# Kernel optimization log

Hardware: AMD Instinct MI355X
Metric: run time of the kernel (lower is better)

Reference implementation:

```python
import jax, jax.numpy as jnp
import numpy as np

B, S, D = 8, 2048, 512


def setup_inputs() -> dict:
    key = jax.random.key(0)
    ks = jax.random.split(key, 8)
    x = jax.random.normal(ks[0], (B, S, D), dtype=jnp.float32)
    mask = jax.random.randint(ks[1], (B, S, 1), 0, 2, dtype=jnp.int32)
    Wq = jax.random.normal(ks[2], (D, D), dtype=jnp.float32) / np.sqrt(D)
    bq = jax.random.normal(ks[3], (D,), dtype=jnp.float32) * 0.01
    Wk = jax.random.normal(ks[4], (D, D), dtype=jnp.float32) / np.sqrt(D)
    bk = jax.random.normal(ks[5], (D,), dtype=jnp.float32) * 0.01
    Wv = jax.random.normal(ks[6], (D, D), dtype=jnp.float32) / np.sqrt(D)
    bv = jax.random.normal(ks[7], (D,), dtype=jnp.float32) * 0.01
    return {"x": x, "mask": mask, "Wq": Wq, "bq": bq, "Wk": Wk, "bk": bk, "Wv": Wv, "bv": bv}


def reference(x, mask, Wq, bq, Wk, bk, Wv, bv):
    # torch Linear: y = x @ W^T + b
    Q = jnp.einsum('bsd,ed->bse', x, Wq) + bq
    K = jnp.einsum('bsd,ed->bse', x, Wk) + bk
    V = jnp.einsum('bsd,ed->bse', x, Wv) + bv
    scale = 1.0 / jnp.sqrt(jnp.asarray(x.shape[-1], dtype=x.dtype))
    scores = jnp.einsum('bqd,bkd->bqk', Q, K) * scale  # [B, S, S]
    attn_mask = jnp.transpose(mask, (0, 2, 1))  # [B, 1, S], broadcasts over queries
    scores = jnp.where(attn_mask == 0, jnp.asarray(-10000.0, dtype=scores.dtype), scores)
    attn = jax.nn.softmax(scores, axis=-1)
    return jnp.einsum('bqk,bkd->bqd', attn, V)
```

## Files before the change

kernel.cpp:

```cpp
#include <hip/hip_runtime.h>
#include <cstddef>

#define BB 8
#define SS 2048
#define DD 512
#define MM (BB * SS)

typedef __attribute__((ext_vector_type(8))) short bf16x8;
typedef __attribute__((ext_vector_type(4))) float f32x4;
typedef __attribute__((ext_vector_type(4))) unsigned short u16x4;

__device__ __forceinline__ f32x4 mfma16(bf16x8 a, bf16x8 b, f32x4 c) {
  return __builtin_amdgcn_mfma_f32_16x16x32_bf16(a, b, c, 0, 0, 0);
}
__device__ __forceinline__ unsigned short f2bf(float f) {
  unsigned int u = __float_as_uint(f);
  u += 0x7fffu + ((u >> 16) & 1u);
  return (unsigned short)(u >> 16);
}
__device__ __forceinline__ void gld16(const void* g, void* l) {
  __builtin_amdgcn_global_load_lds((const __attribute__((address_space(1))) void*)g,
                                   (__attribute__((address_space(3))) void*)l, 16, 0, 0);
}

__global__ void prep_kernel(const float* __restrict__ x, unsigned short* __restrict__ Xb,
                            const float* __restrict__ Wq, const float* __restrict__ Wk,
                            const float* __restrict__ Wv, unsigned short* __restrict__ Wqb,
                            unsigned short* __restrict__ Wkb, unsigned short* __restrict__ Wvb,
                            const int* __restrict__ mask, int* __restrict__ idx,
                            int* __restrict__ nbArr) {
  __shared__ int part[256];
  const int bx = blockIdx.x;
  const int t = threadIdx.x;
  if (bx < 8192) {
    const int i = bx * 256 + t;
    f32x4 v = reinterpret_cast<const f32x4*>(x)[i];
    u16x4 o;
    o[0] = f2bf(v[0]);
    o[1] = f2bf(v[1]);
    o[2] = f2bf(v[2]);
    o[3] = f2bf(v[3]);
    reinterpret_cast<u16x4*>(Xb)[i] = o;
    return;
  }
  if (bx < 8960) {
    const int k = bx - 8192;
    const int which = k >> 8;
    const float* s = which == 0 ? Wq : (which == 1 ? Wk : Wv);
    unsigned short* d = which == 0 ? Wqb : (which == 1 ? Wkb : Wvb);
    const int i = (k & 255) * 256 + t;
    f32x4 v = reinterpret_cast<const f32x4*>(s)[i];
    u16x4 o;
    o[0] = f2bf(v[0]);
    o[1] = f2bf(v[1]);
    o[2] = f2bf(v[2]);
    o[3] = f2bf(v[3]);
    reinterpret_cast<u16x4*>(d)[i] = o;
    return;
  }
  const int b = bx - 8960;
  int m[8], c = 0;
#pragma unroll
  for (int e = 0; e < 8; ++e) {
    m[e] = mask[b * SS + t * 8 + e];
    c += (m[e] != 0);
  }
  int v = c;
  part[t] = v;
  __syncthreads();
  for (int off = 1; off < 256; off <<= 1) {
    int u = (t >= off) ? part[t - off] : 0;
    __syncthreads();
    v += u;
    part[t] = v;
    __syncthreads();
  }
  int base = v - c;
#pragma unroll
  for (int e = 0; e < 8; ++e)
    if (m[e]) idx[b * SS + base++] = t * 8 + e;
  const int nb = part[255];
  if (t == 255) nbArr[b] = nb;
  for (int j = nb + t; j < SS; j += 256) idx[b * SS + j] = 0;
}

__global__ __launch_bounds__(256, 2) void qkv_gemm_kernel(
    const unsigned short* __restrict__ X, const unsigned short* __restrict__ W0,
    const unsigned short* __restrict__ W1, const unsigned short* __restrict__ W2,
    const float* __restrict__ b0, const float* __restrict__ b1,
    const float* __restrict__ b2, unsigned short* __restrict__ O0,
    unsigned short* __restrict__ O1, unsigned short* __restrict__ O2) {
  __shared__ unsigned char a_lds[2][128 * 128];
  __shared__ unsigned char b_lds[2][128 * 128];
  const int tid = threadIdx.x;
  const int w = tid >> 6, l = tid & 63, lr = l & 15, hi = l >> 4;
  const int bid = blockIdx.x;
  const int xcd = bid & 7;
  const int rest = bid >> 3;
  const int j = rest % 12;
  const int mhi = rest / 12;
  const int which = j >> 2;
  const unsigned short* W = which == 0 ? W0 : (which == 1 ? W1 : W2);
  const float* bias = which == 0 ? b0 : (which == 1 ? b1 : b2);
  unsigned short* out = which == 0 ? O0 : (which == 1 ? O1 : O2);
  const float oscale = which == 0 ? 0.044194173824159216f : 1.0f;
  const int m0 = ((mhi << 3) | xcd) * 128;
  const int n0 = (j & 3) * 128;
  const int wm = (w >> 1) * 64, wn = (w & 1) * 64;
  const int srow = l >> 3, gchunk = (l & 7) ^ (srow & 7);

  f32x4 acc[4][4];
#pragma unroll
  for (int mt = 0; mt < 4; ++mt)
#pragma unroll
    for (int nt = 0; nt < 4; ++nt) acc[mt][nt] = (f32x4){0.f, 0.f, 0.f, 0.f};

  const unsigned short* ga = X + (size_t)(m0 + w * 32 + srow) * DD + gchunk * 8;
  const unsigned short* gb = W + (size_t)(n0 + w * 32 + srow) * DD + gchunk * 8;

  for (int k0 = 0; k0 < DD; k0 += 128) {
#pragma unroll
    for (int ii = 0; ii < 4; ++ii) {
      gld16(ga + (size_t)ii * 8 * DD + k0, &a_lds[0][(w * 4 + ii) * 1024]);
      gld16(gb + (size_t)ii * 8 * DD + k0, &b_lds[0][(w * 4 + ii) * 1024]);
      gld16(ga + (size_t)ii * 8 * DD + k0 + 64, &a_lds[1][(w * 4 + ii) * 1024]);
      gld16(gb + (size_t)ii * 8 * DD + k0 + 64, &b_lds[1][(w * 4 + ii) * 1024]);
    }
    __syncthreads();
#pragma unroll
    for (int hf = 0; hf < 2; ++hf) {
#pragma unroll
      for (int dkl = 0; dkl < 2; ++dkl) {
        const int gc = dkl * 4 + hi;
        bf16x8 af[4], bfr[4];
#pragma unroll
        for (int mt = 0; mt < 4; ++mt) {
          const int row = wm + mt * 16 + lr;
          af[mt] = *reinterpret_cast<const bf16x8*>(
              &a_lds[hf][row * 128 + ((gc ^ (row & 7)) * 16)]);
        }
#pragma unroll
        for (int nt = 0; nt < 4; ++nt) {
          const int row = wn + nt * 16 + lr;
          bfr[nt] = *reinterpret_cast<const bf16x8*>(
              &b_lds[hf][row * 128 + ((gc ^ (row & 7)) * 16)]);
        }
#pragma unroll
        for (int mt = 0; mt < 4; ++mt)
#pragma unroll
          for (int nt = 0; nt < 4; ++nt)
            acc[mt][nt] = mfma16(af[mt], bfr[nt], acc[mt][nt]);
      }
    }
    __syncthreads();
  }

#pragma unroll
  for (int nt = 0; nt < 4; ++nt) {
    const int col = n0 + wn + nt * 16 + lr;
    const float bv = bias[col];
#pragma unroll
    for (int mt = 0; mt < 4; ++mt)
#pragma unroll
      for (int r = 0; r < 4; ++r) {
        const int row = m0 + wm + mt * 16 + hi * 4 + r;
        out[(size_t)row * DD + col] = f2bf((acc[mt][nt][r] + bv) * oscale);
      }
  }
}

__global__ void vtrans_kernel(const unsigned short* __restrict__ V,
                              const int* __restrict__ idx, const int* __restrict__ nbArr,
                              unsigned short* __restrict__ VT2) {
  __shared__ unsigned short t[64][72];
  const int b = blockIdx.z;
  const int kt = blockIdx.x;
  const int d0 = blockIdx.y * 64;
  const int tid = threadIdx.x;
  const int c = tid & 63, rg = tid >> 6;
  const int nb = nbArr[b];
#pragma unroll
  for (int i = 0; i < 16; ++i) {
    const int row = rg * 16 + i;
    const int s = kt * 64 + row;
    const int src = s < nb ? idx[b * SS + s] : 0;
    t[row][c] = V[((size_t)b * SS + src) * DD + d0 + c];
  }
  __syncthreads();
#pragma unroll
  for (int i = 0; i < 16; ++i) {
    const int ix = i * 256 + tid;
    const int jj = ix & 7;
    const int dl = (ix >> 3) & 63;
    const int cc = ix >> 9;
    VT2[(((size_t)(b * 32 + kt) * 8 + cc) * 512 + d0 + dl) * 8 + jj] =
        t[cc * 8 + jj][dl];
  }
}

__global__ __launch_bounds__(256, 2) void attn_kernel(
    const unsigned short* __restrict__ Q, const unsigned short* __restrict__ K,
    const unsigned short* __restrict__ VT2, const int* __restrict__ idx,
    const int* __restrict__ nbArr, float* __restrict__ Out,
    float* __restrict__ Apart, float* __restrict__ mlpart) {
  __shared__ unsigned char k_lds[32 * 1024];
  __shared__ unsigned char vt_lds[4 * 512 * 16];
  __shared__ unsigned short pbuf[4][16][32];
  __shared__ int ids[1024];
  const int tid = threadIdx.x;
  const int w = tid >> 6, l = tid & 63, lr = l & 15, hi = l >> 4;
  const int bid = blockIdx.x;
  const int b = bid & 7;
  const int qt = (bid >> 3) >> 1;
  const int sp = (bid >> 3) & 1;
  const int q0 = qt * 64 + w * 16;

  const int nb = nbArr[b];
  const int ntile = (nb + 31) >> 5;
  const int half = (ntile + 1) >> 1;
  const int lo = sp == 0 ? 0 : half;
  const int hi_t = sp == 0 ? half : ntile;
  const int ntl = hi_t - lo;

  const unsigned short* __restrict__ Qb = Q + (size_t)b * SS * DD;
  const unsigned short* __restrict__ Kb = K + (size_t)b * SS * DD;
  const unsigned short* __restrict__ Vb = VT2 + (size_t)b * SS * DD;
  const int* __restrict__ idxb = idx + b * SS;

  for (int j = tid; j < ntl * 32; j += 256) ids[j] = idxb[lo * 32 + j];

  bf16x8 qf[16];
#pragma unroll
  for (int dk = 0; dk < 16; ++dk)
    qf[dk] = *reinterpret_cast<const bf16x8*>(
        &Qb[(size_t)(q0 + lr) * DD + dk * 32 + hi * 8]);

  f32x4 oacc[32];
#pragma unroll
  for (int i = 0; i < 32; ++i) oacc[i] = (f32x4){0.f, 0.f, 0.f, 0.f};
  float mrow[4], lrow[4];
#pragma unroll
  for (int r = 0; r < 4; ++r) {
    mrow[r] = -10000.0f;
    lrow[r] = 0.0f;
  }

  __syncthreads();

  for (int t = lo; t < hi_t; ++t) {
    const int tr = t - lo;
#pragma unroll
    for (int r = 0; r < 8; ++r) {
      const int row = w * 8 + r;
      const int src = ids[tr * 32 + row];
      const int ch = (l & 56) | ((l ^ row) & 7);
      gld16(Kb + (size_t)src * DD + ch * 8, &k_lds[row * 1024]);
    }
    const size_t vbase = ((size_t)((t >> 1) * 8 + (t & 1) * 4 + w) * 512);
#pragma unroll
    for (int g = 0; g < 8; ++g)
      gld16(Vb + (vbase + g * 64 + l) * 8, &vt_lds[(w * 512 + g * 64) * 16]);

    asm volatile("s_waitcnt vmcnt(8)" ::: "memory");
    __builtin_amdgcn_s_barrier();

    f32x4 sacc[2];
#pragma unroll
    for (int nt = 0; nt < 2; ++nt) sacc[nt] = (f32x4){0.f, 0.f, 0.f, 0.f};
    __builtin_amdgcn_s_setprio(1);
#pragma unroll
    for (int dk = 0; dk < 16; ++dk) {
#pragma unroll
      for (int nt = 0; nt < 2; ++nt) {
        const int row = nt * 16 + lr;
        const int c = dk * 4 + hi;
        bf16x8 bk = *reinterpret_cast<const bf16x8*>(
            &k_lds[row * 1024 + ((c & ~7) | ((c ^ row) & 7)) * 16]);
        sacc[nt] = mfma16(qf[dk], bk, sacc[nt]);
      }
    }
    __builtin_amdgcn_s_setprio(0);

    float s[2][4];
#pragma unroll
    for (int nt = 0; nt < 2; ++nt) {
      const int j = t * 32 + nt * 16 + lr;
      const bool ok = j < nb;
#pragma unroll
      for (int r = 0; r < 4; ++r)
        s[nt][r] = ok ? sacc[nt][r] : -10000.0f;
    }

    float mx[4];
    float need = -1e30f;
#pragma unroll
    for (int r = 0; r < 4; ++r) {
      float m2 = fmaxf(s[0][r], s[1][r]);
#pragma unroll
      for (int off = 1; off < 16; off <<= 1) m2 = fmaxf(m2, __shfl_xor(m2, off));
      mx[r] = m2;
      need = fmaxf(need, m2 - mrow[r]);
    }
    if (__any(need > 8.0f)) {
#pragma unroll
      for (int r = 0; r < 4; ++r) {
        const float mnew = fmaxf(mrow[r], mx[r]);
        const float alpha = __expf(mrow[r] - mnew);
        mrow[r] = mnew;
        lrow[r] *= alpha;
#pragma unroll
        for (int nt2 = 0; nt2 < 32; ++nt2) oacc[nt2][r] *= alpha;
      }
    }
    float rs[4] = {0.f, 0.f, 0.f, 0.f};
#pragma unroll
    for (int nt = 0; nt < 2; ++nt)
#pragma unroll
      for (int r = 0; r < 4; ++r) {
        float p = __expf(s[nt][r] - mrow[r]);
        s[nt][r] = p;
        rs[r] += p;
      }
#pragma unroll
    for (int r = 0; r < 4; ++r) {
      float tt = rs[r];
#pragma unroll
      for (int off = 1; off < 16; off <<= 1) tt += __shfl_xor(tt, off);
      lrow[r] += tt;
    }

#pragma unroll
    for (int nt = 0; nt < 2; ++nt)
#pragma unroll
      for (int r = 0; r < 4; ++r) {
        const int col = nt * 16 + lr;
        pbuf[w][hi * 4 + r][(((col >> 3) ^ hi) << 3) | (col & 7)] =
            f2bf(s[nt][r]);
      }
    bf16x8 pf = *reinterpret_cast<const bf16x8*>(
        &pbuf[w][lr][(hi ^ (lr >> 2)) << 3]);

    asm volatile("s_waitcnt vmcnt(0)" ::: "memory");
    __builtin_amdgcn_s_barrier();

    __builtin_amdgcn_s_setprio(1);
#pragma unroll
    for (int nt2 = 0; nt2 < 32; ++nt2) {
      bf16x8 v0 = *reinterpret_cast<const bf16x8*>(
          &vt_lds[(hi * 512 + nt2 * 16 + lr) * 16]);
      oacc[nt2] = mfma16(pf, v0, oacc[nt2]);
    }
    __builtin_amdgcn_s_setprio(0);
    __syncthreads();
  }

  float* Ap = sp == 0 ? Out : Apart;
#pragma unroll
  for (int nt2 = 0; nt2 < 32; ++nt2)
#pragma unroll
    for (int r = 0; r < 4; ++r)
      Ap[((size_t)b * SS + q0 + hi * 4 + r) * DD + nt2 * 16 + lr] = oacc[nt2][r];
  if (lr == 0) {
#pragma unroll
    for (int r = 0; r < 4; ++r) {
      const size_t row = (size_t)sp * MM + b * SS + q0 + hi * 4 + r;
      mlpart[row * 2 + 0] = mrow[r];
      mlpart[row * 2 + 1] = lrow[r];
    }
  }
}

__global__ void combine_kernel(float* __restrict__ Out, const float* __restrict__ Apart,
                               const float* __restrict__ mlpart) {
  const int gid = blockIdx.x * 256 + threadIdx.x;
  const int row = gid >> 7;
  const float m1 = mlpart[(size_t)row * 2 + 0];
  const float l1 = mlpart[(size_t)row * 2 + 1];
  const float m2 = mlpart[((size_t)MM + row) * 2 + 0];
  const float l2 = mlpart[((size_t)MM + row) * 2 + 1];
  const float m = fmaxf(m1, m2);
  const float w1 = __expf(m1 - m), w2 = __expf(m2 - m);
  const float inv = 1.0f / (w1 * l1 + w2 * l2);
  f32x4 a1 = reinterpret_cast<f32x4*>(Out)[gid];
  f32x4 a2 = reinterpret_cast<const f32x4*>(Apart)[gid];
  f32x4 o;
#pragma unroll
  for (int e = 0; e < 4; ++e) o[e] = (w1 * a1[e] + w2 * a2[e]) * inv;
  reinterpret_cast<f32x4*>(Out)[gid] = o;
}

extern "C" void kernel_launch(void* const* d_in, const int* in_sizes, int n_in,
                              void* d_out, int out_size, void* d_ws, size_t ws_size,
                              hipStream_t stream) {
  const float* x = (const float*)d_in[0];
  const int* mask = (const int*)d_in[1];
  const float* Wq = (const float*)d_in[2];
  const float* bq = (const float*)d_in[3];
  const float* Wk = (const float*)d_in[4];
  const float* bk = (const float*)d_in[5];
  const float* Wv = (const float*)d_in[6];
  const float* bv = (const float*)d_in[7];
  float* out = (float*)d_out;

  char* ws = (char*)d_ws;
  const size_t MB = 1024 * 1024;
  unsigned short* Qb = (unsigned short*)(ws);
  unsigned short* Kb = (unsigned short*)(ws + 16 * MB);
  unsigned short* VT2b = (unsigned short*)(ws + 32 * MB);
  unsigned short* Xb = (unsigned short*)(ws + 48 * MB);
  unsigned short* Vb = (unsigned short*)(ws + 64 * MB);
  float* Apart = (float*)(ws + 48 * MB);
  unsigned short* Wqb = (unsigned short*)(ws + 80 * MB);
  unsigned short* Wkb = Wqb + 512 * 512;
  unsigned short* Wvb = Wkb + 512 * 512;
  int* idx = (int*)(ws + 82 * MB);
  int* nbArr = (int*)(ws + 82 * MB + 65536);
  float* mlpart = (float*)(ws + 82 * MB + 128 * 1024);

  prep_kernel<<<8968, 256, 0, stream>>>(x, Xb, Wq, Wk, Wv, Wqb, Wkb, Wvb, mask, idx,
                                        nbArr);

  qkv_gemm_kernel<<<1536, 256, 0, stream>>>(Xb, Wqb, Wkb, Wvb, bq, bk, bv, Qb, Kb, Vb);

  vtrans_kernel<<<dim3(SS / 64, DD / 64, BB), 256, 0, stream>>>(Vb, idx, nbArr, VT2b);

  attn_kernel<<<512, 256, 0, stream>>>(Qb, Kb, VT2b, idx, nbArr, out, Apart, mlpart);

  combine_kernel<<<(MM * DD / 4) / 256, 256, 0, stream>>>(out, Apart, mlpart);
}
```

Before: 228.1 us.

## Fuse Q/K/V projections per block to reuse X tile across three weights

Each QKV GEMM block now computes the same 128x128 output tile for all three weight matrices, loading the X tile once and reusing it against Wq, Wk and Wv. The grid drops from 1536 to 512 blocks and the K-step shrinks from 128 to 64 so LDS stays at 64KB. The aim is to cut redundant X loads from global memory. In exchange, accumulator registers triple (192 floats per thread), which risks spills or lower occupancy under launch_bounds(256,2), and there are fewer blocks to spread across the CUs.

```diff
diff --git a/kernel.cpp b/kernel.cpp
--- a/kernel.cpp
+++ b/kernel.cpp
@@ -90,82 +90,89 @@
     const float* __restrict__ b0, const float* __restrict__ b1,
     const float* __restrict__ b2, unsigned short* __restrict__ O0,
     unsigned short* __restrict__ O1, unsigned short* __restrict__ O2) {
-  __shared__ unsigned char a_lds[2][128 * 128];
-  __shared__ unsigned char b_lds[2][128 * 128];
+  __shared__ unsigned char a_lds[16 * 1024];
+  __shared__ unsigned char b_lds[3][16 * 1024];
   const int tid = threadIdx.x;
   const int w = tid >> 6, l = tid & 63, lr = l & 15, hi = l >> 4;
   const int bid = blockIdx.x;
   const int xcd = bid & 7;
-  const int rest = bid >> 3;
-  const int j = rest % 12;
-  const int mhi = rest / 12;
-  const int which = j >> 2;
-  const unsigned short* W = which == 0 ? W0 : (which == 1 ? W1 : W2);
-  const float* bias = which == 0 ? b0 : (which == 1 ? b1 : b2);
-  unsigned short* out = which == 0 ? O0 : (which == 1 ? O1 : O2);
-  const float oscale = which == 0 ? 0.044194173824159216f : 1.0f;
-  const int m0 = ((mhi << 3) | xcd) * 128;
-  const int n0 = (j & 3) * 128;
+  const int q = bid >> 3;
+  const int nI = q & 3;
+  const int mhi = q >> 2;
+  const int m0 = (mhi * 8 + xcd) * 128;
+  const int n0 = nI * 128;
   const int wm = (w >> 1) * 64, wn = (w & 1) * 64;
   const int srow = l >> 3, gchunk = (l & 7) ^ (srow & 7);
 
-  f32x4 acc[4][4];
-#pragma unroll
-  for (int mt = 0; mt < 4; ++mt)
-#pragma unroll
-    for (int nt = 0; nt < 4; ++nt) acc[mt][nt] = (f32x4){0.f, 0.f, 0.f, 0.f};
+  f32x4 acc[3][4][4];
+#pragma unroll
+  for (int mat = 0; mat < 3; ++mat)
+#pragma unroll
+    for (int mt = 0; mt < 4; ++mt)
+#pragma unroll
+      for (int nt = 0; nt < 4; ++nt) acc[mat][mt][nt] = (f32x4){0.f, 0.f, 0.f, 0.f};
 
   const unsigned short* ga = X + (size_t)(m0 + w * 32 + srow) * DD + gchunk * 8;
-  const unsigned short* gb = W + (size_t)(n0 + w * 32 + srow) * DD + gchunk * 8;
-
-  for (int k0 = 0; k0 < DD; k0 += 128) {
+  const unsigned short* gb0 = W0 + (size_t)(n0 + w * 32 + srow) * DD + gchunk * 8;
+  const unsigned short* gb1 = W1 + (size_t)(n0 + w * 32 + srow) * DD + gchunk * 8;
+  const unsigned short* gb2 = W2 + (size_t)(n0 + w * 32 + srow) * DD + gchunk * 8;
+
+  for (int k0 = 0; k0 < DD; k0 += 64) {
 #pragma unroll
     for (int ii = 0; ii < 4; ++ii) {
-      gld16(ga + (size_t)ii * 8 * DD + k0, &a_lds[0][(w * 4 + ii) * 1024]);
-      gld16(gb + (size_t)ii * 8 * DD + k0, &b_lds[0][(w * 4 + ii) * 1024]);
-      gld16(ga + (size_t)ii * 8 * DD + k0 + 64, &a_lds[1][(w * 4 + ii) * 1024]);
-      gld16(gb + (size_t)ii * 8 * DD + k0 + 64, &b_lds[1][(w * 4 + ii) * 1024]);
+      const int dst = (w * 4 + ii) * 1024;
+      gld16(ga + (size_t)ii * 8 * DD + k0, &a_lds[dst]);
+      gld16(gb0 + (size_t)ii * 8 * DD + k0, &b_lds[0][dst]);
+      gld16(gb1 + (size_t)ii * 8 * DD + k0, &b_lds[1][dst]);
+      gld16(gb2 + (size_t)ii * 8 * DD + k0, &b_lds[2][dst]);
     }
     __syncthreads();
 #pragma unroll
-    for (int hf = 0; hf < 2; ++hf) {
-#pragma unroll
-      for (int dkl = 0; dkl < 2; ++dkl) {
-        const int gc = dkl * 4 + hi;
-        bf16x8 af[4], bfr[4];
-#pragma unroll
-        for (int mt = 0; mt < 4; ++mt) {
-          const int row = wm + mt * 16 + lr;
-          af[mt] = *reinterpret_cast<const bf16x8*>(
-              &a_lds[hf][row * 128 + ((gc ^ (row & 7)) * 16)]);
-        }
+    for (int dkl = 0; dkl < 2; ++dkl) {
+      const int gc = dkl * 4 + hi;
+      bf16x8 af[4];
+#pragma unroll
+      for (int mt = 0; mt < 4; ++mt) {
+        const int row = wm + mt * 16 + lr;
+        af[mt] = *reinterpret_cast<const bf16x8*>(
+            &a_lds[row * 128 + ((gc ^ (row & 7)) * 16)]);
+      }
+#pragma unroll
+      for (int mat = 0; mat < 3; ++mat) {
+        bf16x8 bfr[4];
 #pragma unroll
         for (int nt = 0; nt < 4; ++nt) {
           const int row = wn + nt * 16 + lr;
           bfr[nt] = *reinterpret_cast<const bf16x8*>(
-              &b_lds[hf][row * 128 + ((gc ^ (row & 7)) * 16)]);
+              &b_lds[mat][row * 128 + ((gc ^ (row & 7)) * 16)]);
         }
 #pragma unroll
         for (int mt = 0; mt < 4; ++mt)
 #pragma unroll
           for (int nt = 0; nt < 4; ++nt)
-            acc[mt][nt] = mfma16(af[mt], bfr[nt], acc[mt][nt]);
+            acc[mat][mt][nt] = mfma16(af[mt], bfr[nt], acc[mat][mt][nt]);
       }
     }
     __syncthreads();
   }
 
 #pragma unroll
-  for (int nt = 0; nt < 4; ++nt) {
-    const int col = n0 + wn + nt * 16 + lr;
-    const float bv = bias[col];
-#pragma unroll
-    for (int mt = 0; mt < 4; ++mt)
-#pragma unroll
-      for (int r = 0; r < 4; ++r) {
-        const int row = m0 + wm + mt * 16 + hi * 4 + r;
-        out[(size_t)row * DD + col] = f2bf((acc[mt][nt][r] + bv) * oscale);
-      }
+  for (int mat = 0; mat < 3; ++mat) {
+    const float* bias = mat == 0 ? b0 : (mat == 1 ? b1 : b2);
+    unsigned short* out = mat == 0 ? O0 : (mat == 1 ? O1 : O2);
+    const float oscale = mat == 0 ? 0.044194173824159216f : 1.0f;
+#pragma unroll
+    for (int nt = 0; nt < 4; ++nt) {
+      const int col = n0 + wn + nt * 16 + lr;
+      const float bv = bias[col];
+#pragma unroll
+      for (int mt = 0; mt < 4; ++mt)
+#pragma unroll
+        for (int r = 0; r < 4; ++r) {
+          const int row = m0 + wm + mt * 16 + hi * 4 + r;
+          out[(size_t)row * DD + col] = f2bf((acc[mat][mt][nt][r] + bv) * oscale);
+        }
+    }
   }
 }
 
@@ -420,7 +427,7 @@
   prep_kernel<<<8968, 256, 0, stream>>>(x, Xb, Wq, Wk, Wv, Wqb, Wkb, Wvb, mask, idx,
                                         nbArr);
 
-  qkv_gemm_kernel<<<1536, 256, 0, stream>>>(Xb, Wqb, Wkb, Wvb, bq, bk, bv, Qb, Kb, Vb);
+  qkv_gemm_kernel<<<512, 256, 0, stream>>>(Xb, Wqb, Wkb, Wvb, bq, bk, bv, Qb, Kb, Vb);
 
   vtrans_kernel<<<dim3(SS / 64, DD / 64, BB), 256, 0, stream>>>(Vb, idx, nbArr, VT2b);
 
```

Result: no change. 223.9 us (-1.8%).
